# Kernel tuning notes

Hardware: AMD Instinct MI355X
Metric: run time of the kernel (lower is better)

Reference implementation:

```python
import jax, jax.numpy as jnp
import numpy as np

B = 2048        # batch size
D = 512         # emb_dim
N_ATTRS = 512   # number of attribute operators
N_OBJS = 2000   # object vocabulary


def setup_inputs() -> dict:
    key = jax.random.key(0)
    k1, k2, k3, k4 = jax.random.split(key, 4)
    attrs = jax.random.randint(k1, (B,), 0, N_ATTRS, dtype=jnp.int64 if jax.config.jax_enable_x64 else jnp.int32)
    objs = jax.random.randint(k2, (B,), 0, N_OBJS, dtype=jnp.int64 if jax.config.jax_enable_x64 else jnp.int32)
    # per-attribute operator matrices (initialized as identity in the torch
    # module; random here to exercise the math) and object embedding table
    attr_ops = jax.random.normal(k3, (N_ATTRS, D, D), dtype=jnp.float32) * 0.02
    obj_emb = jax.random.normal(k4, (N_OBJS, D), dtype=jnp.float32)
    return {"attrs": attrs, "objs": objs, "attr_ops": attr_ops, "obj_emb": obj_emb}


def reference(attrs, objs, attr_ops, obj_emb):
    # compose(): obj_rep = obj_embedder(objs)            [B, D]
    obj_rep = jnp.take(obj_emb, objs, axis=0)
    # gather per-sample operator matrix (torch: Python-loop stack over ParameterList)
    ops = jnp.take(attr_ops, attrs, axis=0)              # [B, D, D]
    # apply_ops(): bmm(ops, rep.unsqueeze(2)).squeeze(2) then ReLU
    out = jnp.einsum('bij,bj->bi', ops, obj_rep)         # [B, D]
    return jax.nn.relu(out)
```

## Files before the change

kernel.cpp:

```cpp
#include <hip/hip_runtime.h>


constexpr int B_SZ    = 2048;
constexpr int D_SZ    = 512;
constexpr int N_ATTRS = 512;
constexpr int SPLIT   = 2;
constexpr int ROWS_PER_BLOCK = D_SZ / SPLIT;
constexpr int THREADS = 256;

__device__ __forceinline__ float wave_sum(float p) {
#pragma unroll
  for (int off = 32; off; off >>= 1) p += __shfl_xor(p, off);
  return p;
}

template <int NS>
__device__ __forceinline__ void do_chunk(
    const int* __restrict__ s_idx, int s0, int cnt,
    const int* __restrict__ objs,
    const float* __restrict__ M,
    const float* __restrict__ obj_emb,
    float* __restrict__ out,
    int rowbase, int lane) {
  const int nthis = min(cnt - s0, NS);

  float4 ra[NS], rb[NS];
  int bi[NS];
#pragma unroll
  for (int s = 0; s < NS; ++s) {
    int si = s0 + s;
    if (si >= cnt) si = s0;
    const int b = s_idx[si];
    bi[s] = b;
    const float* rep = obj_emb + (size_t)objs[b] * D_SZ;
    ra[s] = *(const float4*)(rep + 4 * lane);
    rb[s] = *(const float4*)(rep + D_SZ / 2 + 4 * lane);
  }

  float res[NS];
#pragma unroll 4
  for (int r = 0; r < 64; ++r) {
    const float* Mr = M + (size_t)(rowbase + r) * D_SZ;
    const float4 ma = *(const float4*)(Mr + 4 * lane);
    const float4 mb = *(const float4*)(Mr + D_SZ / 2 + 4 * lane);
#pragma unroll
    for (int s = 0; s < NS; ++s) {
      float p = ma.x * ra[s].x + ma.y * ra[s].y + ma.z * ra[s].z + ma.w * ra[s].w
              + mb.x * rb[s].x + mb.y * rb[s].y + mb.z * rb[s].z + mb.w * rb[s].w;
      p = wave_sum(p);
      if (lane == r) res[s] = p;
    }
  }

#pragma unroll
  for (int s = 0; s < NS; ++s) {
    if (s < nthis)
      out[(size_t)bi[s] * D_SZ + rowbase + lane] = fmaxf(res[s], 0.0f);
  }
}

__global__ __launch_bounds__(THREADS) void attr_op_kernel(
    const int* __restrict__ attrs, const int* __restrict__ objs,
    const float* __restrict__ attr_ops, const float* __restrict__ obj_emb,
    float* __restrict__ out) {
  __shared__ int s_idx[B_SZ];
  __shared__ int s_cnt;

  const int attr = blockIdx.x >> 1;
  const int half = blockIdx.x & 1;

  if (threadIdx.x == 0) s_cnt = 0;
  __syncthreads();

  for (int b = threadIdx.x; b < B_SZ; b += THREADS) {
    if (attrs[b] == attr) {
      int p = atomicAdd(&s_cnt, 1);
      s_idx[p] = b;
    }
  }
  __syncthreads();
  const int cnt = s_cnt;
  if (cnt == 0) return;

  const int lane = threadIdx.x & 63;
  const int wave = threadIdx.x >> 6;
  const int rowbase = half * ROWS_PER_BLOCK + wave * 64;
  const float* __restrict__ M = attr_ops + (size_t)attr * D_SZ * D_SZ;

  for (int s0 = 0; s0 < cnt; s0 += 8) {
    if (cnt - s0 > 4)
      do_chunk<8>(s_idx, s0, cnt, objs, M, obj_emb, out, rowbase, lane);
    else
      do_chunk<4>(s_idx, s0, cnt, objs, M, obj_emb, out, rowbase, lane);
  }
}

extern "C" void kernel_launch(void* const* d_in, const int* in_sizes, int n_in,
                              void* d_out, int out_size, void* d_ws, size_t ws_size,
                              hipStream_t stream) {
  const int*   attrs    = (const int*)d_in[0];
  const int*   objs     = (const int*)d_in[1];
  const float* attr_ops = (const float*)d_in[2];
  const float* obj_emb  = (const float*)d_in[3];
  float*       out      = (float*)d_out;

  attr_op_kernel<<<N_ATTRS * SPLIT, THREADS, 0, stream>>>(
      attrs, objs, attr_ops, obj_emb, out);
}
```

Before: 883.8 us.

## Split each wave into four 16-lane groups, one sample per group

The work mapping changes from a full 64-lane wave doing each row dot product for up to 8 samples to four 16-lane quarter-waves, each handling one sample and loading the whole 512-element row per lane group. This cuts the reduction from a 6-step wave shuffle per sample per row to a 4-step shuffle within 16 lanes, and lowers register pressure by keeping one embedding vector per lane instead of eight. In exchange, each M row is loaded by all four groups, which relies on cache hits, and only 4 samples share each row load instead of 8.

```diff
diff --git a/kernel.cpp b/kernel.cpp
--- a/kernel.cpp
+++ b/kernel.cpp
@@ -5,59 +5,7 @@
 constexpr int D_SZ    = 512;
 constexpr int N_ATTRS = 512;
 constexpr int SPLIT   = 2;
-constexpr int ROWS_PER_BLOCK = D_SZ / SPLIT;
 constexpr int THREADS = 256;
-
-__device__ __forceinline__ float wave_sum(float p) {
-#pragma unroll
-  for (int off = 32; off; off >>= 1) p += __shfl_xor(p, off);
-  return p;
-}
-
-template <int NS>
-__device__ __forceinline__ void do_chunk(
-    const int* __restrict__ s_idx, int s0, int cnt,
-    const int* __restrict__ objs,
-    const float* __restrict__ M,
-    const float* __restrict__ obj_emb,
-    float* __restrict__ out,
-    int rowbase, int lane) {
-  const int nthis = min(cnt - s0, NS);
-
-  float4 ra[NS], rb[NS];
-  int bi[NS];
-#pragma unroll
-  for (int s = 0; s < NS; ++s) {
-    int si = s0 + s;
-    if (si >= cnt) si = s0;
-    const int b = s_idx[si];
-    bi[s] = b;
-    const float* rep = obj_emb + (size_t)objs[b] * D_SZ;
-    ra[s] = *(const float4*)(rep + 4 * lane);
-    rb[s] = *(const float4*)(rep + D_SZ / 2 + 4 * lane);
-  }
-
-  float res[NS];
-#pragma unroll 4
-  for (int r = 0; r < 64; ++r) {
-    const float* Mr = M + (size_t)(rowbase + r) * D_SZ;
-    const float4 ma = *(const float4*)(Mr + 4 * lane);
-    const float4 mb = *(const float4*)(Mr + D_SZ / 2 + 4 * lane);
-#pragma unroll
-    for (int s = 0; s < NS; ++s) {
-      float p = ma.x * ra[s].x + ma.y * ra[s].y + ma.z * ra[s].z + ma.w * ra[s].w
-              + mb.x * rb[s].x + mb.y * rb[s].y + mb.z * rb[s].z + mb.w * rb[s].w;
-      p = wave_sum(p);
-      if (lane == r) res[s] = p;
-    }
-  }
-
-#pragma unroll
-  for (int s = 0; s < NS; ++s) {
-    if (s < nthis)
-      out[(size_t)bi[s] * D_SZ + rowbase + lane] = fmaxf(res[s], 0.0f);
-  }
-}
 
 __global__ __launch_bounds__(THREADS) void attr_op_kernel(
     const int* __restrict__ attrs, const int* __restrict__ objs,
@@ -84,14 +32,59 @@
 
   const int lane = threadIdx.x & 63;
   const int wave = threadIdx.x >> 6;
-  const int rowbase = half * ROWS_PER_BLOCK + wave * 64;
+  const int c = lane & 15;
+  const int q = lane >> 4;
+  const int rowbase = half * (D_SZ / SPLIT) + wave * 64;
   const float* __restrict__ M = attr_ops + (size_t)attr * D_SZ * D_SZ;
 
-  for (int s0 = 0; s0 < cnt; s0 += 8) {
-    if (cnt - s0 > 4)
-      do_chunk<8>(s_idx, s0, cnt, objs, M, obj_emb, out, rowbase, lane);
-    else
-      do_chunk<4>(s_idx, s0, cnt, objs, M, obj_emb, out, rowbase, lane);
+  for (int s0 = 0; s0 < cnt; s0 += 4) {
+    int si = s0 + q;
+    const bool live = (si < cnt);
+    if (!live) si = s0;
+    const int b = s_idx[si];
+    const float* rep = obj_emb + (size_t)objs[b] * D_SZ;
+
+    float4 va[4], vb[4];
+#pragma unroll
+    for (int p = 0; p < 4; ++p) {
+      va[p] = *(const float4*)(rep + p * 128 + c * 8);
+      vb[p] = *(const float4*)(rep + p * 128 + c * 8 + 4);
+    }
+
+    float res[4];
+#pragma unroll
+    for (int i = 0; i < 4; ++i) {
+      res[i] = 0.0f;
+#pragma unroll 4
+      for (int rr = 0; rr < 16; ++rr) {
+        const float* Mr = M + (size_t)(rowbase + i * 16 + rr) * D_SZ;
+        float a0 = 0.f, a1 = 0.f, a2 = 0.f, a3 = 0.f;
+#pragma unroll
+        for (int p = 0; p < 4; ++p) {
+          const float4 ma = *(const float4*)(Mr + p * 128 + c * 8);
+          const float4 mb = *(const float4*)(Mr + p * 128 + c * 8 + 4);
+          float t = (p & 1) ? a1 : a0;
+          t += ma.x * va[p].x + ma.y * va[p].y + ma.z * va[p].z + ma.w * va[p].w;
+          if (p & 1) a1 = t; else a0 = t;
+          float u = (p & 1) ? a3 : a2;
+          u += mb.x * vb[p].x + mb.y * vb[p].y + mb.z * vb[p].z + mb.w * vb[p].w;
+          if (p & 1) a3 = u; else a2 = u;
+        }
+        float sum = (a0 + a1) + (a2 + a3);
+        sum += __shfl_xor(sum, 1);
+        sum += __shfl_xor(sum, 2);
+        sum += __shfl_xor(sum, 4);
+        sum += __shfl_xor(sum, 8);
+        res[i] = (c == rr) ? sum : res[i];
+      }
+    }
+
+    if (live) {
+      float* o = out + (size_t)b * D_SZ + rowbase + c;
+#pragma unroll
+      for (int i = 0; i < 4; ++i)
+        o[i * 16] = fmaxf(res[i], 0.0f);
+    }
   }
 }
 
```

Result: faster. 852.7 us (-3.5%).
